# Kernel tuning notes

Measured on AMD Instinct MI355X. Metric: run time of the kernel, lower is better.

## Reference

```python
import jax, jax.numpy as jnp
import numpy as np

BN_EPS = 1e-5

def _bn(y, g, b, m, v):
    # inference-mode BatchNorm2d over channel axis 1
    scale = g / jnp.sqrt(v + BN_EPS)
    return (y - m[None, :, None, None]) * scale[None, :, None, None] + b[None, :, None, None]

def setup_inputs() -> dict:
    key = jax.random.key(0)
    ks = jax.random.split(key, 16)
    b, c, h, w = 4, 64, 256, 512
    kc = 32
    return {
        "x": jax.random.normal(ks[0], (b, c, h, w), dtype=jnp.float32),
        "Wq": jax.random.normal(ks[1], (kc, c), dtype=jnp.float32) * 0.05,
        "bnq_g": jax.random.uniform(ks[2], (kc,), dtype=jnp.float32),
        "bnq_b": jax.random.normal(ks[3], (kc,), dtype=jnp.float32) * 0.1,
        "bnq_m": jax.random.normal(ks[4], (kc,), dtype=jnp.float32) * 0.1,
        "bnq_v": jax.random.uniform(ks[5], (kc,), dtype=jnp.float32) + 0.5,
        "Wk": jax.random.normal(ks[6], (kc, c), dtype=jnp.float32) * 0.05,
        "bnk_g": jax.random.uniform(ks[7], (kc,), dtype=jnp.float32),
        "bnk_b": jax.random.normal(ks[8], (kc,), dtype=jnp.float32) * 0.1,
        "bnk_m": jax.random.normal(ks[9], (kc,), dtype=jnp.float32) * 0.1,
        "bnk_v": jax.random.uniform(ks[10], (kc,), dtype=jnp.float32) + 0.5,
        "Wv": jax.random.normal(ks[11], (c, c), dtype=jnp.float32) * 0.05,
        "bv": jax.random.normal(ks[12], (c,), dtype=jnp.float32) * 0.1,
        "gamma": jax.random.normal(ks[13], (1,), dtype=jnp.float32) * 0.1,
    }

def reference(x, Wq, bnq_g, bnq_b, bnq_m, bnq_v, Wk, bnk_g, bnk_b, bnk_m, bnk_v, Wv, bv, gamma):
    # x: [b,c,h,w]. Vertical (height-axis) attention, independent per (batch, column).
    q = _bn(jnp.einsum('kc,bchw->bkhw', Wq, x), bnq_g, bnq_b, bnq_m, bnq_v)  # [b,kc,h,w]
    k = _bn(jnp.einsum('kc,bchw->bkhw', Wk, x), bnk_g, bnk_b, bnk_m, bnk_v)  # [b,kc,h,w]
    # score1 = Q[b,w,h,kc] @ K[b,w,kc,h] -> [b,w,h,h]
    score = jnp.einsum('bkhw,bkgw->bwhg', q, k)
    attn = jax.nn.softmax(score, axis=-1)  # softmax over key height g
    v = jnp.einsum('dc,bchw->bdhw', Wv, x) + bv[None, :, None, None]  # [b,c,h,w]
    buf = jnp.einsum('bwhg,bdgw->bdhw', attn, v)  # [b,c,h,w]
    return gamma * buf + x  # out_add branch
```

## Files before the change

kernel.cpp:

```cpp
#include <hip/hip_runtime.h>
#include <hip/hip_bf16.h>

#define BB 4
#define CC 64
#define HH 256
#define WW 512
#define KCC 32
#define PLANE (HH*WW)

typedef __attribute__((ext_vector_type(8))) __bf16 bf16x8;
typedef __attribute__((ext_vector_type(4))) __bf16 bf16x4;
typedef __attribute__((ext_vector_type(2))) __bf16 bf16x2;
typedef __attribute__((ext_vector_type(4))) float floatx4;

__device__ __forceinline__ float bf2f(unsigned short u) {
    union { unsigned v; float f; } x; x.v = ((unsigned)u) << 16; return x.f;
}

__global__ __launch_bounds__(256, 4)
void proj_kernel(const float* __restrict__ x,
                 const float* __restrict__ Wq, const float* __restrict__ Wk,
                 const float* __restrict__ Wv, const float* __restrict__ bv,
                 const float* __restrict__ bnq_g, const float* __restrict__ bnq_b,
                 const float* __restrict__ bnq_m, const float* __restrict__ bnq_v,
                 const float* __restrict__ bnk_g, const float* __restrict__ bnk_b,
                 const float* __restrict__ bnk_m, const float* __restrict__ bnk_v,
                 unsigned short* __restrict__ Qb, unsigned short* __restrict__ Kb,
                 unsigned short* __restrict__ Vb)
{
    __shared__ __align__(16) unsigned short sX[8 * 256 * 8];
    __shared__ __align__(16) unsigned short sY[4][16 * 40];
    __shared__ float sScale[128], sBias[128];

    const int tid  = threadIdx.x;
    const int lane = tid & 63, wv = tid >> 6;
    const int quad = lane >> 4, lr = lane & 15;
    const int bid  = blockIdx.x;
    const int b = bid >> 9, chunk = bid & 511;
    const int h = chunk >> 1, w0 = (chunk & 1) << 8;

    if (tid < 128) {
        float s, bia;
        if (tid < 32)      { s = bnq_g[tid] * rsqrtf(bnq_v[tid] + 1e-5f); bia = bnq_b[tid] - bnq_m[tid] * s; }
        else if (tid < 64) { int i = tid - 32; s = bnk_g[i] * rsqrtf(bnk_v[i] + 1e-5f); bia = bnk_b[i] - bnk_m[i] * s; }
        else               { s = 1.f; bia = bv[tid - 64]; }
        sScale[tid] = s; sBias[tid] = bia;
    }

    {
        const float* xb = x + (size_t)b * CC * PLANE + h * WW + w0 + tid;
#pragma unroll
        for (int cc = 0; cc < 8; ++cc) {
            bf16x8 v;
#pragma unroll
            for (int j = 0; j < 8; ++j) v[j] = (__bf16)xb[(size_t)(cc * 8 + j) * PLANE];
            *(bf16x8*)&sX[(cc * 256 + tid) * 8] = v;
        }
    }
    __syncthreads();

    const float* Wsrc = (wv == 0) ? Wq : (wv == 1) ? Wk : (Wv + (wv - 2) * 32 * CC);
    bf16x8 wf[2][2];
#pragma unroll
    for (int mt = 0; mt < 2; ++mt)
#pragma unroll
        for (int ks = 0; ks < 2; ++ks) {
            const float* p = Wsrc + (mt * 16 + lr) * CC + ks * 32 + quad * 8;
            bf16x8 v;
#pragma unroll
            for (int j = 0; j < 8; ++j) v[j] = (__bf16)p[j];
            wf[mt][ks] = v;
        }
    float s8[2][4], b8[2][4];
#pragma unroll
    for (int mt = 0; mt < 2; ++mt)
#pragma unroll
        for (int i = 0; i < 4; ++i) {
            int chn = wv * 32 + mt * 16 + quad * 4 + i;
            s8[mt][i] = sScale[chn]; b8[mt][i] = sBias[chn];
        }

    unsigned short* sYw = sY[wv];
    const int p2 = lane >> 2, seg = lane & 3;

    for (int nt = 0; nt < 16; ++nt) {
        bf16x8 xb0 = *(const bf16x8*)&sX[((0 + quad) * 256 + nt * 16 + lr) * 8];
        bf16x8 xb1 = *(const bf16x8*)&sX[((4 + quad) * 256 + nt * 16 + lr) * 8];
#pragma unroll
        for (int mt = 0; mt < 2; ++mt) {
            floatx4 acc = {0.f, 0.f, 0.f, 0.f};
            acc = __builtin_amdgcn_mfma_f32_16x16x32_bf16(wf[mt][0], xb0, acc, 0, 0, 0);
            acc = __builtin_amdgcn_mfma_f32_16x16x32_bf16(wf[mt][1], xb1, acc, 0, 0, 0);
            bf16x4 y;
#pragma unroll
            for (int i = 0; i < 4; ++i) y[i] = (__bf16)(acc[i] * s8[mt][i] + b8[mt][i]);
            *(bf16x4*)&sYw[lr * 40 + mt * 16 + quad * 4] = y;
        }
        uint4 v = *(const uint4*)&sYw[p2 * 40 + seg * 8];
        int w_ = w0 + nt * 16 + p2;
        if (wv == 0)      *(uint4*)&Qb[(size_t)((b * WW + w_) * HH + h) * KCC + seg * 8] = v;
        else if (wv == 1) *(uint4*)&Kb[(size_t)((b * WW + w_) * HH + h) * KCC + seg * 8] = v;
        else              *(uint4*)&Vb[(size_t)((b * WW + w_) * HH + h) * CC + (wv - 2) * 32 + seg * 8] = v;
    }
}

__global__ __launch_bounds__(256, 2)
void attn_kernel(const unsigned short* __restrict__ Qb,
                 const unsigned short* __restrict__ Kb,
                 const unsigned short* __restrict__ Vb,
                 const float* __restrict__ gamma,
                 unsigned short* __restrict__ Ob)
{
    __shared__ __align__(16) unsigned short sV[64 * 264];
    __shared__ __align__(16) unsigned short sU[4][2560];
    __shared__ float sL[256];

    const int tid = threadIdx.x, lane = tid & 63, wv = tid >> 6;
    const int quad = lane >> 4, lr = lane & 15;
    const int col = blockIdx.x;

    const unsigned short* Qg = Qb + (size_t)col * HH * KCC;
    const unsigned short* Kg = Kb + (size_t)col * HH * KCC;
    const unsigned short* Vg = Vb + (size_t)col * HH * CC;

    bf16x8 qf[4], kf[16];
#pragma unroll
    for (int ht = 0; ht < 4; ++ht)
        qf[ht] = *(const bf16x8*)&Qg[(wv * 64 + ht * 16 + lr) * KCC + quad * 8];
#pragma unroll
    for (int gt = 0; gt < 16; ++gt)
        kf[gt] = *(const bf16x8*)&Kg[(gt * 16 + lr) * KCC + quad * 8];

    unsigned short* sVp = &sU[0][0];
    for (int half = 0; half < 2; ++half) {
#pragma unroll
        for (int it = 0; it < 2; ++it) {
            int idx = it * 256 + tid;
            int gr = idx >> 2, sg = idx & 3;
            (void)gr; (void)sg;
        }
        {
#pragma unroll
            for (int it = 0; it < 4; ++it) {
                int idx = it * 256 + tid;
                int gr = idx >> 3, sg = idx & 7;
                uint4 v = *(const uint4*)&Vg[(size_t)(half * 128 + gr) * CC + sg * 8];
                *(uint4*)&sVp[gr * CC + sg * 8] = v;
            }
        }
        __syncthreads();
        {
            int d = tid & 63, gq = tid >> 6;
#pragma unroll
            for (int j = 0; j < 16; ++j) {
                int grel = gq * 32 + 2 * j;
                __bf16 v0 = *(const __bf16*)&sVp[grel * CC + d];
                __bf16 v1 = *(const __bf16*)&sVp[(grel + 1) * CC + d];
                bf16x2 pp = {v0, v1};
                *(bf16x2*)&sV[d * 264 + half * 128 + grel] = pp;
            }
        }
        __syncthreads();
    }

    const float gm = gamma[0];
    floatx4 O[4][4];
#pragma unroll
    for (int a = 0; a < 4; ++a)
#pragma unroll
        for (int dd = 0; dd < 4; ++dd) O[a][dd] = (floatx4){0.f, 0.f, 0.f, 0.f};
    float lpart[4] = {0.f, 0.f, 0.f, 0.f};

    unsigned short* sPw = sU[wv];
    const floatx4 zed = {0.f, 0.f, 0.f, 0.f};

#pragma unroll
    for (int ch = 0; ch < 8; ++ch) {
#pragma unroll
        for (int gt = 0; gt < 2; ++gt) {
#pragma unroll
            for (int ht = 0; ht < 4; ++ht) {
                floatx4 s = __builtin_amdgcn_mfma_f32_16x16x32_bf16(kf[ch * 2 + gt], qf[ht], zed, 0, 0, 0);
                float p0 = __expf(s[0]), p1 = __expf(s[1]), p2 = __expf(s[2]), p3 = __expf(s[3]);
                lpart[ht] += (p0 + p1) + (p2 + p3);
                bf16x2 pa = {(__bf16)p0, (__bf16)p1};
                bf16x2 pb = {(__bf16)p2, (__bf16)p3};
                int base = (ht * 16 + lr) * 40 + gt * 16 + quad * 4;
                *(bf16x2*)&sPw[base]     = pa;
                *(bf16x2*)&sPw[base + 2] = pb;
            }
        }
        bf16x8 paf[4];
#pragma unroll
        for (int ht = 0; ht < 4; ++ht)
            paf[ht] = *(const bf16x8*)&sPw[(ht * 16 + lr) * 40 + quad * 8];
#pragma unroll
        for (int dt = 0; dt < 4; ++dt) {
            bf16x8 vf = *(const bf16x8*)&sV[(dt * 16 + lr) * 264 + ch * 32 + quad * 8];
#pragma unroll
            for (int ht = 0; ht < 4; ++ht)
                O[ht][dt] = __builtin_amdgcn_mfma_f32_16x16x32_bf16(paf[ht], vf, O[ht][dt], 0, 0, 0);
        }
    }

#pragma unroll
    for (int ht = 0; ht < 4; ++ht) {
        float l = lpart[ht];
        l += __shfl_xor(l, 16, 64);
        l += __shfl_xor(l, 32, 64);
        if (lane < 16) sL[wv * 64 + ht * 16 + lane] = gm / l;
    }

    unsigned short* sOw = sU[wv];
#pragma unroll
    for (int half = 0; half < 2; ++half) {
#pragma unroll
        for (int htl = 0; htl < 2; ++htl) {
            int ht = half * 2 + htl;
            float f0 = sL[wv * 64 + ht * 16 + quad * 4 + 0];
            float f1 = sL[wv * 64 + ht * 16 + quad * 4 + 1];
            float f2 = sL[wv * 64 + ht * 16 + quad * 4 + 2];
            float f3 = sL[wv * 64 + ht * 16 + quad * 4 + 3];
#pragma unroll
            for (int dt = 0; dt < 4; ++dt) {
                floatx4 o = O[ht][dt];
                int cbase = dt * 16 + lr;
                *(__bf16*)&sOw[(htl * 16 + quad * 4 + 0) * 72 + cbase] = (__bf16)(o[0] * f0);
                *(__bf16*)&sOw[(htl * 16 + quad * 4 + 1) * 72 + cbase] = (__bf16)(o[1] * f1);
                *(__bf16*)&sOw[(htl * 16 + quad * 4 + 2) * 72 + cbase] = (__bf16)(o[2] * f2);
                *(__bf16*)&sOw[(htl * 16 + quad * 4 + 3) * 72 + cbase] = (__bf16)(o[3] * f3);
            }
        }
#pragma unroll
        for (int it = 0; it < 4; ++it) {
            int idx = it * 64 + lane;
            int hr = idx >> 3, sg = idx & 7;
            uint4 v = *(const uint4*)&sOw[hr * 72 + sg * 8];
            *(uint4*)&Ob[(size_t)(col * HH + wv * 64 + half * 32 + hr) * CC + sg * 8] = v;
        }
    }
}

__global__ __launch_bounds__(256)
void add_kernel(const unsigned short* __restrict__ Ob,
                const float* __restrict__ x,
                float* __restrict__ out)
{
    __shared__ __align__(16) unsigned short sT[64 * 72];
    const int tid = threadIdx.x;
    const int bid = blockIdx.x;
    const int b = bid >> 11, rem = bid & 2047, h = rem >> 3, w0 = (rem & 7) << 6;

#pragma unroll
    for (int it = 0; it < 2; ++it) {
        int idx = it * 256 + tid;
        int tw = idx >> 3, sg = idx & 7;
        uint4 v = *(const uint4*)&Ob[(size_t)((b * WW + w0 + tw) * HH + h) * CC + sg * 8];
        *(uint4*)&sT[tw * 72 + sg * 8] = v;
    }
    __syncthreads();

    const int d = tid >> 2, ws = tid & 3;
    const size_t base = ((size_t)(b * CC + d)) * PLANE + h * WW + w0 + ws * 16;
    const float* xp = x + base;
    float* op = out + base;
#pragma unroll
    for (int k = 0; k < 4; ++k) {
        float4 xv = *(const float4*)&xp[k * 4];
        float4 r;
        r.x = bf2f(sT[(ws * 16 + k * 4 + 0) * 72 + d]) + xv.x;
        r.y = bf2f(sT[(ws * 16 + k * 4 + 1) * 72 + d]) + xv.y;
        r.z = bf2f(sT[(ws * 16 + k * 4 + 2) * 72 + d]) + xv.z;
        r.w = bf2f(sT[(ws * 16 + k * 4 + 3) * 72 + d]) + xv.w;
        *(float4*)&op[k * 4] = r;
    }
}

#define KSTR 40
#define VSTR 72
__device__ __forceinline__ float bflo(unsigned u) { union { unsigned v; float f; } x; x.v = u << 16; return x.f; }
__device__ __forceinline__ float bfhi(unsigned u) { union { unsigned v; float f; } x; x.v = u & 0xffff0000u; return x.f; }

__global__ __launch_bounds__(256, 1)
void vattn_fused(const float* __restrict__ x,
                 const float* __restrict__ Wq,
                 const float* __restrict__ bnq_g, const float* __restrict__ bnq_b,
                 const float* __restrict__ bnq_m, const float* __restrict__ bnq_v,
                 const float* __restrict__ Wk,
                 const float* __restrict__ bnk_g, const float* __restrict__ bnk_b,
                 const float* __restrict__ bnk_m, const float* __restrict__ bnk_v,
                 const float* __restrict__ Wv, const float* __restrict__ bv,
                 const float* __restrict__ gamma,
                 float* __restrict__ out)
{
    __shared__ __align__(16) __hip_bfloat16 sK[HH * KSTR];
    __shared__ __align__(16) __hip_bfloat16 sV2[HH * VSTR];
    const int t = threadIdx.x;
    const int bw = blockIdx.x;
    const int b = bw / WW, w = bw % WW;
    const size_t plane = (size_t)HH * WW;
    const float* xp = x + (size_t)b * CC * plane + (size_t)t * WW + w;
    float xr[CC];
#pragma unroll
    for (int c = 0; c < CC; ++c) xr[c] = xp[(size_t)c * plane];
    float qr[KCC];
#pragma unroll
    for (int j = 0; j < KCC; ++j) {
        float aq = 0.f, ak = 0.f;
#pragma unroll
        for (int c = 0; c < CC; ++c) { aq += Wq[j * CC + c] * xr[c]; ak += Wk[j * CC + c] * xr[c]; }
        const float sq = bnq_g[j] * rsqrtf(bnq_v[j] + 1e-5f);
        const float sk = bnk_g[j] * rsqrtf(bnk_v[j] + 1e-5f);
        qr[j] = (aq - bnq_m[j]) * sq + bnq_b[j];
        sK[t * KSTR + j] = __float2bfloat16((ak - bnk_m[j]) * sk + bnk_b[j]);
    }
#pragma unroll
    for (int d = 0; d < CC; ++d) {
        float av = bv[d];
#pragma unroll
        for (int c = 0; c < CC; ++c) av += Wv[d * CC + c] * xr[c];
        sV2[t * VSTR + d] = __float2bfloat16(av);
    }
    __syncthreads();
    float o[CC];
#pragma unroll
    for (int d = 0; d < CC; ++d) o[d] = 0.f;
    float l = 0.f;
    for (int g = 0; g < HH; ++g) {
        const uint4* kp = (const uint4*)(sK + g * KSTR);
        float s = 0.f;
#pragma unroll
        for (int i = 0; i < 4; ++i) {
            const uint4 kk = kp[i];
            s += bflo(kk.x) * qr[i * 8 + 0] + bfhi(kk.x) * qr[i * 8 + 1]
               + bflo(kk.y) * qr[i * 8 + 2] + bfhi(kk.y) * qr[i * 8 + 3]
               + bflo(kk.z) * qr[i * 8 + 4] + bfhi(kk.z) * qr[i * 8 + 5]
               + bflo(kk.w) * qr[i * 8 + 6] + bfhi(kk.w) * qr[i * 8 + 7];
        }
        const float p = __expf(s);
        l += p;
        const uint4* vp = (const uint4*)(sV2 + g * VSTR);
#pragma unroll
        for (int i = 0; i < 8; ++i) {
            const uint4 vv = vp[i];
            o[i * 8 + 0] += p * bflo(vv.x); o[i * 8 + 1] += p * bfhi(vv.x);
            o[i * 8 + 2] += p * bflo(vv.y); o[i * 8 + 3] += p * bfhi(vv.y);
            o[i * 8 + 4] += p * bflo(vv.z); o[i * 8 + 5] += p * bfhi(vv.z);
            o[i * 8 + 6] += p * bflo(vv.w); o[i * 8 + 7] += p * bfhi(vv.w);
        }
    }
    const float gm = gamma[0];
    const float rl = 1.f / l;
    float* op = out + (size_t)b * CC * plane + (size_t)t * WW + w;
#pragma unroll
    for (int d = 0; d < CC; ++d) op[(size_t)d * plane] = gm * (o[d] * rl) + xr[d];
}

extern "C" void kernel_launch(void* const* d_in, const int* in_sizes, int n_in,
                              void* d_out, int out_size, void* d_ws, size_t ws_size,
                              hipStream_t stream) {
    const float* x     = (const float*)d_in[0];
    const float* Wq    = (const float*)d_in[1];
    const float* bnq_g = (const float*)d_in[2];
    const float* bnq_b = (const float*)d_in[3];
    const float* bnq_m = (const float*)d_in[4];
    const float* bnq_v = (const float*)d_in[5];
    const float* Wk    = (const float*)d_in[6];
    const float* bnk_g = (const float*)d_in[7];
    const float* bnk_b = (const float*)d_in[8];
    const float* bnk_m = (const float*)d_in[9];
    const float* bnk_v = (const float*)d_in[10];
    const float* Wv    = (const float*)d_in[11];
    const float* bv    = (const float*)d_in[12];
    const float* gamma = (const float*)d_in[13];
    float* out = (float*)d_out;

    const size_t need = 201326592;
    if (ws_size >= need) {
        unsigned short* Qb = (unsigned short*)d_ws;
        unsigned short* Kb = Qb + 16777216;
        unsigned short* Vb = Kb + 16777216;
        unsigned short* Ob = Vb + 33554432;
        hipLaunchKernelGGL(proj_kernel, dim3(2048), dim3(256), 0, stream,
                           x, Wq, Wk, Wv, bv,
                           bnq_g, bnq_b, bnq_m, bnq_v,
                           bnk_g, bnk_b, bnk_m, bnk_v,
                           Qb, Kb, Vb);
        hipLaunchKernelGGL(attn_kernel, dim3(2048), dim3(256), 0, stream,
                           Qb, Kb, Vb, gamma, Ob);
        hipLaunchKernelGGL(add_kernel, dim3(8192), dim3(256), 0, stream,
                           Ob, x, out);
    } else {
        hipLaunchKernelGGL(vattn_fused, dim3(BB * WW), dim3(HH), 0, stream,
                           x, Wq, bnq_g, bnq_b, bnq_m, bnq_v,
                           Wk, bnk_g, bnk_b, bnk_m, bnk_v,
                           Wv, bv, gamma, out);
    }
}
```

Measured before the change: 473.7 us.

## Split attention per column across eight waves and repack V layout in LDS

The attention kernel now runs with 512 threads per block, so each of eight waves handles 32 query rows instead of 64. This halves per-wave accumulator and Q-fragment registers, which allows higher occupancy. V is transposed into a packed 8-element-group layout in LDS so each MFMA B-operand is a contiguous 16-byte read. Register pressure drops, but every wave still holds all 16 K fragments, so K register loads and exp work per block are duplicated across twice as many waves.

Measured after the change: 428.8 us. -9.5%, faster.

```diff
diff --git a/kernel.cpp b/kernel.cpp
--- a/kernel.cpp
+++ b/kernel.cpp
@@ -104,15 +104,15 @@
     }
 }
 
-__global__ __launch_bounds__(256, 2)
+__global__ __launch_bounds__(512, 4)
 void attn_kernel(const unsigned short* __restrict__ Qb,
                  const unsigned short* __restrict__ Kb,
                  const unsigned short* __restrict__ Vb,
                  const float* __restrict__ gamma,
                  unsigned short* __restrict__ Ob)
 {
-    __shared__ __align__(16) unsigned short sV[64 * 264];
-    __shared__ __align__(16) unsigned short sU[4][2560];
+    __shared__ __align__(16) unsigned short sVf[16384];
+    __shared__ __align__(16) unsigned short sP[8][1280];
     __shared__ float sL[256];
 
     const int tid = threadIdx.x, lane = tid & 63, wv = tid >> 6;
@@ -123,55 +123,45 @@
     const unsigned short* Kg = Kb + (size_t)col * HH * KCC;
     const unsigned short* Vg = Vb + (size_t)col * HH * CC;
 
-    bf16x8 qf[4], kf[16];
-#pragma unroll
-    for (int ht = 0; ht < 4; ++ht)
-        qf[ht] = *(const bf16x8*)&Qg[(wv * 64 + ht * 16 + lr) * KCC + quad * 8];
+    bf16x8 qf[2], kf[16];
+#pragma unroll
+    for (int ht = 0; ht < 2; ++ht)
+        qf[ht] = *(const bf16x8*)&Qg[(wv * 32 + ht * 16 + lr) * KCC + quad * 8];
 #pragma unroll
     for (int gt = 0; gt < 16; ++gt)
         kf[gt] = *(const bf16x8*)&Kg[(gt * 16 + lr) * KCC + quad * 8];
 
-    unsigned short* sVp = &sU[0][0];
+    unsigned short* sVp = &sP[0][0];
     for (int half = 0; half < 2; ++half) {
 #pragma unroll
         for (int it = 0; it < 2; ++it) {
-            int idx = it * 256 + tid;
-            int gr = idx >> 2, sg = idx & 3;
-            (void)gr; (void)sg;
-        }
-        {
-#pragma unroll
-            for (int it = 0; it < 4; ++it) {
-                int idx = it * 256 + tid;
-                int gr = idx >> 3, sg = idx & 7;
-                uint4 v = *(const uint4*)&Vg[(size_t)(half * 128 + gr) * CC + sg * 8];
-                *(uint4*)&sVp[gr * CC + sg * 8] = v;
-            }
+            int idx = it * 512 + tid;
+            int gr = idx >> 3, sg = idx & 7;
+            *(uint4*)&sVp[gr * CC + sg * 8] =
+                *(const uint4*)&Vg[(size_t)(half * 128 + gr) * CC + sg * 8];
         }
         __syncthreads();
-        {
-            int d = tid & 63, gq = tid >> 6;
-#pragma unroll
-            for (int j = 0; j < 16; ++j) {
-                int grel = gq * 32 + 2 * j;
-                __bf16 v0 = *(const __bf16*)&sVp[grel * CC + d];
-                __bf16 v1 = *(const __bf16*)&sVp[(grel + 1) * CC + d];
-                bf16x2 pp = {v0, v1};
-                *(bf16x2*)&sV[d * 264 + half * 128 + grel] = pp;
-            }
+#pragma unroll
+        for (int it = 0; it < 2; ++it) {
+            int id = it * 512 + tid;
+            int go = id >> 6, d = id & 63;
+            bf16x8 v;
+#pragma unroll
+            for (int j = 0; j < 8; ++j)
+                ((unsigned short*)&v)[j] = sVp[(go * 8 + j) * CC + d];
+            *(bf16x8*)&sVf[((half * 16 + go) * 64 + d) * 8] = v;
         }
         __syncthreads();
     }
 
-    const float gm = gamma[0];
-    floatx4 O[4][4];
-#pragma unroll
-    for (int a = 0; a < 4; ++a)
+    floatx4 O[2][4];
+#pragma unroll
+    for (int a = 0; a < 2; ++a)
 #pragma unroll
         for (int dd = 0; dd < 4; ++dd) O[a][dd] = (floatx4){0.f, 0.f, 0.f, 0.f};
-    float lpart[4] = {0.f, 0.f, 0.f, 0.f};
-
-    unsigned short* sPw = sU[wv];
+    float lpart[2] = {0.f, 0.f};
+
+    unsigned short* sPw = sP[wv];
     const floatx4 zed = {0.f, 0.f, 0.f, 0.f};
 
 #pragma unroll
@@ -179,7 +169,7 @@
 #pragma unroll
         for (int gt = 0; gt < 2; ++gt) {
 #pragma unroll
-            for (int ht = 0; ht < 4; ++ht) {
+            for (int ht = 0; ht < 2; ++ht) {
                 floatx4 s = __builtin_amdgcn_mfma_f32_16x16x32_bf16(kf[ch * 2 + gt], qf[ht], zed, 0, 0, 0);
                 float p0 = __expf(s[0]), p1 = __expf(s[1]), p2 = __expf(s[2]), p3 = __expf(s[3]);
                 lpart[ht] += (p0 + p1) + (p2 + p3);
@@ -190,53 +180,49 @@
                 *(bf16x2*)&sPw[base + 2] = pb;
             }
         }
-        bf16x8 paf[4];
-#pragma unroll
-        for (int ht = 0; ht < 4; ++ht)
+        bf16x8 paf[2];
+#pragma unroll
+        for (int ht = 0; ht < 2; ++ht)
             paf[ht] = *(const bf16x8*)&sPw[(ht * 16 + lr) * 40 + quad * 8];
 #pragma unroll
         for (int dt = 0; dt < 4; ++dt) {
-            bf16x8 vf = *(const bf16x8*)&sV[(dt * 16 + lr) * 264 + ch * 32 + quad * 8];
-#pragma unroll
-            for (int ht = 0; ht < 4; ++ht)
+            bf16x8 vf = *(const bf16x8*)&sVf[((ch * 4 + quad) * 64 + dt * 16 + lr) * 8];
+#pragma unroll
+            for (int ht = 0; ht < 2; ++ht)
                 O[ht][dt] = __builtin_amdgcn_mfma_f32_16x16x32_bf16(paf[ht], vf, O[ht][dt], 0, 0, 0);
         }
     }
 
-#pragma unroll
-    for (int ht = 0; ht < 4; ++ht) {
+    const float gm = gamma[0];
+#pragma unroll
+    for (int ht = 0; ht < 2; ++ht) {
         float l = lpart[ht];
         l += __shfl_xor(l, 16, 64);
         l += __shfl_xor(l, 32, 64);
-        if (lane < 16) sL[wv * 64 + ht * 16 + lane] = gm / l;
-    }
-
-    unsigned short* sOw = sU[wv];
-#pragma unroll
-    for (int half = 0; half < 2; ++half) {
-#pragma unroll
-        for (int htl = 0; htl < 2; ++htl) {
-            int ht = half * 2 + htl;
-            float f0 = sL[wv * 64 + ht * 16 + quad * 4 + 0];
-            float f1 = sL[wv * 64 + ht * 16 + quad * 4 + 1];
-            float f2 = sL[wv * 64 + ht * 16 + quad * 4 + 2];
-            float f3 = sL[wv * 64 + ht * 16 + quad * 4 + 3];
-#pragma unroll
-            for (int dt = 0; dt < 4; ++dt) {
-                floatx4 o = O[ht][dt];
-                int cbase = dt * 16 + lr;
-                *(__bf16*)&sOw[(htl * 16 + quad * 4 + 0) * 72 + cbase] = (__bf16)(o[0] * f0);
-                *(__bf16*)&sOw[(htl * 16 + quad * 4 + 1) * 72 + cbase] = (__bf16)(o[1] * f1);
-                *(__bf16*)&sOw[(htl * 16 + quad * 4 + 2) * 72 + cbase] = (__bf16)(o[2] * f2);
-                *(__bf16*)&sOw[(htl * 16 + quad * 4 + 3) * 72 + cbase] = (__bf16)(o[3] * f3);
-            }
-        }
-#pragma unroll
-        for (int it = 0; it < 4; ++it) {
+        if (lane < 16) sL[wv * 32 + ht * 16 + lane] = gm / l;
+    }
+
+#pragma unroll
+    for (int ht = 0; ht < 2; ++ht) {
+        float f0 = sL[wv * 32 + ht * 16 + quad * 4 + 0];
+        float f1 = sL[wv * 32 + ht * 16 + quad * 4 + 1];
+        float f2 = sL[wv * 32 + ht * 16 + quad * 4 + 2];
+        float f3 = sL[wv * 32 + ht * 16 + quad * 4 + 3];
+#pragma unroll
+        for (int dt = 0; dt < 4; ++dt) {
+            floatx4 o = O[ht][dt];
+            int cb = dt * 16 + lr;
+            *(__bf16*)&sPw[(quad * 4 + 0) * 72 + cb] = (__bf16)(o[0] * f0);
+            *(__bf16*)&sPw[(quad * 4 + 1) * 72 + cb] = (__bf16)(o[1] * f1);
+            *(__bf16*)&sPw[(quad * 4 + 2) * 72 + cb] = (__bf16)(o[2] * f2);
+            *(__bf16*)&sPw[(quad * 4 + 3) * 72 + cb] = (__bf16)(o[3] * f3);
+        }
+#pragma unroll
+        for (int it = 0; it < 2; ++it) {
             int idx = it * 64 + lane;
             int hr = idx >> 3, sg = idx & 7;
-            uint4 v = *(const uint4*)&sOw[hr * 72 + sg * 8];
-            *(uint4*)&Ob[(size_t)(col * HH + wv * 64 + half * 32 + hr) * CC + sg * 8] = v;
+            uint4 v = *(const uint4*)&sPw[hr * 72 + sg * 8];
+            *(uint4*)&Ob[(size_t)(col * HH + wv * 32 + ht * 16 + hr) * CC + sg * 8] = v;
         }
     }
 }
@@ -386,7 +372,7 @@
                            bnq_g, bnq_b, bnq_m, bnq_v,
                            bnk_g, bnk_b, bnk_m, bnk_v,
                            Qb, Kb, Vb);
-        hipLaunchKernelGGL(attn_kernel, dim3(2048), dim3(256), 0, stream,
+        hipLaunchKernelGGL(attn_kernel, dim3(2048), dim3(512), 0, stream,
                            Qb, Kb, Vb, gamma, Ob);
         hipLaunchKernelGGL(add_kernel, dim3(8192), dim3(256), 0, stream,
                            Ob, x, out);
```
